# Optimization experiments

Hardware: AMD Instinct MI355X
Metric: run time of the kernel (lower is better)

Reference implementation:

```python
import jax, jax.numpy as jnp
import numpy as np

N, E, G, R = 65536, 524288, 1024, 512
D_IN, H, R_FEAT, NH, HD = 7, 128, 25, 4, 32
EPS = 1e-5


def setup_inputs() -> dict:
    key = jax.random.key(0)
    ks = jax.random.split(key, 16)
    f = lambda i, shape, s: jax.random.normal(ks[i], shape, jnp.float32) * s
    return {
        "x": jax.random.normal(ks[0], (N, D_IN), jnp.float32),
        "edge_index": jax.random.randint(ks[1], (2, E), 0, N),
        "batch": jnp.repeat(jnp.arange(G), N // G),  # 64 atoms per graph, sorted
        "per_residue_features": jax.random.normal(ks[2], (R, R_FEAT), jnp.float32),
        # GCN layer weights (PyG GCNConv: x @ W then normalized aggregation, + bias)
        "W0": f(3, (D_IN, H), 0.3), "b0": jnp.zeros(H, jnp.float32),
        "W1": f(4, (H, H), 0.1), "b1": jnp.zeros(H, jnp.float32),
        "W2": f(5, (H, H), 0.1), "b2": jnp.zeros(H, jnp.float32),
        # BatchNorm (eval mode, running stats)
        "bn_gamma": jnp.ones((3, H), jnp.float32),
        "bn_beta": jnp.zeros((3, H), jnp.float32),
        "bn_mean": f(6, (3, H), 0.1),
        "bn_var": jax.random.uniform(ks[7], (3, H), jnp.float32) + 0.5,
        # residue projection
        "res_W": f(8, (R_FEAT, H), 0.2), "res_b": jnp.zeros(H, jnp.float32),
        # MultiheadAttention packed in-proj (rows: q, k, v) and out-proj
        "in_W": f(9, (3 * H, H), 0.08), "in_b": jnp.zeros(3 * H, jnp.float32),
        "out_W": f(10, (H, H), 0.08), "out_b": jnp.zeros(H, jnp.float32),
        # classifier 128 -> 64 -> 1
        "cls_W1": f(11, (H, 64), 0.1), "cls_b1": jnp.zeros(64, jnp.float32),
        "cls_W2": f(12, (64, 1), 0.1), "cls_b2": jnp.zeros(1, jnp.float32),
    }


def reference(x, edge_index, batch, per_residue_features,
              W0, b0, W1, b1, W2, b2,
              bn_gamma, bn_beta, bn_mean, bn_var,
              res_W, res_b, in_W, in_b, out_W, out_b,
              cls_W1, cls_b1, cls_W2, cls_b2):
    src, dst = edge_index[0], edge_index[1]
    # GCN symmetric norm with self-loops: deg[i] = 1 + in-degree(i)
    deg = jnp.ones(N, x.dtype).at[dst].add(1.0)
    dinv = jax.lax.rsqrt(deg)
    enorm = (dinv[src] * dinv[dst])[:, None]      # [E,1]
    self_norm = (dinv * dinv)[:, None]            # [N,1]

    def gcn_bn_relu(h, W, b, i):
        m = h @ W                                  # [N,H]
        agg = m * self_norm
        agg = agg.at[dst].add(m[src] * enorm) + b
        y = bn_gamma[i] * (agg - bn_mean[i]) * jax.lax.rsqrt(bn_var[i] + EPS) + bn_beta[i]
        return jax.nn.relu(y)  # dropout is identity at inference

    h = gcn_bn_relu(x, W0, b0, 0)
    h = gcn_bn_relu(h, W1, b1, 1)
    h = gcn_bn_relu(h, W2, b2, 2)

    # shared residue KV (same for every graph) -> fused attention over all nodes
    res = per_residue_features @ res_W + res_b     # [R,H]
    Wq, Wk, Wv = jnp.split(in_W, 3, axis=0)
    bq, bk, bv = jnp.split(in_b, 3)
    q = (h @ Wq.T + bq).reshape(N, NH, HD)
    k = (res @ Wk.T + bk).reshape(R, NH, HD)
    v = (res @ Wv.T + bv).reshape(R, NH, HD)
    scores = jnp.einsum('nhd,rhd->nhr', q, k) / np.float32(np.sqrt(HD))
    attn = jax.nn.softmax(scores, axis=-1)         # [N,NH,R]
    o = jnp.einsum('nhr,rhd->nhd', attn, v).reshape(N, H)
    o = o @ out_W.T + out_b                        # [N,H]

    # per-graph mean pool (segment mean over batch ids)
    counts = jnp.zeros(G, o.dtype).at[batch].add(1.0)
    pooled = jnp.zeros((G, H), o.dtype).at[batch].add(o) / counts[:, None]

    hid = jax.nn.relu(pooled @ cls_W1 + cls_b1)
    logits = (hid @ cls_W2 + cls_b2)[:, 0]         # [G]
    return logits
```

## Files before the change

### kernel.cpp

```cpp
#include <hip/hip_runtime.h>
#include <math.h>

#define N_NODES 65536
#define N_EDGES 524288
#define N_GRAPHS 1024
#define H 128
#define R_RES 512
#define NH 4
#define HD 32
#define D_IN 7
#define EPS 1e-5f

typedef __attribute__((ext_vector_type(8))) short short8;
typedef __attribute__((ext_vector_type(4))) short short4v;
typedef __attribute__((ext_vector_type(4))) float f32x4;
typedef __attribute__((ext_vector_type(4))) unsigned uint4v;
typedef __attribute__((ext_vector_type(2))) unsigned uint2v;
typedef __attribute__((ext_vector_type(4))) unsigned short us4;

#if __has_builtin(__builtin_amdgcn_exp2f)
#define EXP2F __builtin_amdgcn_exp2f
#else
#define EXP2F exp2f
#endif
#if __has_builtin(__builtin_amdgcn_rcpf)
#define RCPF __builtin_amdgcn_rcpf
#else
#define RCPF(x) (1.0f/(x))
#endif

__device__ __forceinline__ f32x4 mfma_k16(short4v a, short4v b, f32x4 c){
#if defined(__HIP_DEVICE_COMPILE__)
  return __builtin_amdgcn_mfma_f32_16x16x16bf16_1k(a, b, c, 0, 0, 0);
#else
  (void)a; (void)b; return c;
#endif
}

__device__ __forceinline__ unsigned short rnd_bf16(float f){
  return (unsigned short)((__builtin_bit_cast(unsigned, f) + 0x8000u) >> 16);
}
__device__ __forceinline__ unsigned pk_bf16(float lo, float hi){
  unsigned a = __builtin_bit_cast(unsigned, lo) + 0x8000u;
  unsigned b = __builtin_bit_cast(unsigned, hi) + 0x8000u;
  return __builtin_amdgcn_perm(b, a, 0x07060302u);
}
__device__ __forceinline__ float bflo(unsigned u){ return __builtin_bit_cast(float, u << 16); }
__device__ __forceinline__ float bfhi(unsigned u){ return __builtin_bit_cast(float, u & 0xFFFF0000u); }

__device__ __forceinline__ void acc8(float* a, uint4v u, float wgt){
  a[0]=fmaf(bflo(u.x),wgt,a[0]); a[1]=fmaf(bfhi(u.x),wgt,a[1]);
  a[2]=fmaf(bflo(u.y),wgt,a[2]); a[3]=fmaf(bfhi(u.y),wgt,a[3]);
  a[4]=fmaf(bflo(u.z),wgt,a[4]); a[5]=fmaf(bfhi(u.z),wgt,a[5]);
  a[6]=fmaf(bflo(u.w),wgt,a[6]); a[7]=fmaf(bfhi(u.w),wgt,a[7]);
}

__global__ __launch_bounds__(256) void k_count(const int* __restrict__ dst, int* __restrict__ cnt, int E){
  int e = blockIdx.x*256 + threadIdx.x;
  if (e < E) atomicAdd(&cnt[dst[e]], 1);
}

__global__ __launch_bounds__(256) void k_part(const int* __restrict__ cnt, int* __restrict__ part){
  int i = blockIdx.x*256 + threadIdx.x;
  int v = cnt[i];
  #pragma unroll
  for (int off=1; off<64; off<<=1) v += __shfl_xor(v, off);
  __shared__ int red[4];
  if ((threadIdx.x & 63) == 0) red[threadIdx.x >> 6] = v;
  __syncthreads();
  if (threadIdx.x == 0) part[blockIdx.x] = red[0]+red[1]+red[2]+red[3];
}

__global__ __launch_bounds__(256) void k_scanp(int* __restrict__ part){
  __shared__ int s[256];
  int t = threadIdx.x;
  int v = part[t];
  s[t] = v;
  __syncthreads();
  for (int off=1; off<256; off<<=1){
    int u = (t >= off) ? s[t-off] : 0;
    __syncthreads();
    s[t] += u;
    __syncthreads();
  }
  part[t] = s[t] - v;
}

__global__ __launch_bounds__(256) void k_apply(const int* __restrict__ cnt, const int* __restrict__ part,
      int* __restrict__ csr_off, int* __restrict__ cursor, float* __restrict__ dinv){
  __shared__ int s[256];
  int b = blockIdx.x, t = threadIdx.x;
  int i = b*256 + t;
  int c = cnt[i];
  s[t] = c;
  __syncthreads();
  for (int off=1; off<256; off<<=1){
    int u = (t >= off) ? s[t-off] : 0;
    __syncthreads();
    s[t] += u;
    __syncthreads();
  }
  int o0 = part[b] + s[t] - c;
  csr_off[i] = o0;
  cursor[i] = o0;
  dinv[i] = rsqrtf(1.0f + (float)c);
  if (i == N_NODES-1) csr_off[N_NODES] = N_EDGES;
}

__global__ __launch_bounds__(256) void k_fill(const int* __restrict__ src, const int* __restrict__ dst,
      const float* __restrict__ dinv, int* __restrict__ cursor, int2* __restrict__ csr_ev, int E){
  int e = blockIdx.x*256 + threadIdx.x;
  if (e >= E) return;
  int s = src[e], d = dst[e];
  int p = atomicAdd(&cursor[d], 1);
  int2 rec;
  rec.x = s;
  rec.y = __builtin_bit_cast(int, dinv[s]*dinv[d]);
  csr_ev[p] = rec;
}

__global__ __launch_bounds__(256) void k_lin0(const float* __restrict__ x, const float* __restrict__ W0,
                                              unsigned short* __restrict__ out){
  int gid = blockIdx.x*256 + threadIdx.x;
  int l = threadIdx.x & 63;
  int n = __builtin_amdgcn_readfirstlane(gid >> 6);
  float a0 = 0.0f, a1 = 0.0f;
  #pragma unroll
  for (int k=0;k<D_IN;k++){
    float xv = x[(long)n*D_IN + k];
    float2 wv = *(const float2*)(W0 + k*H + 2*l);
    a0 = fmaf(xv, wv.x, a0); a1 = fmaf(xv, wv.y, a1);
  }
  *(unsigned*)(out + (long)n*H + 2*l) = pk_bf16(a0, a1);
}

__global__ __launch_bounds__(256) void k_gemm_mfma(const unsigned short* __restrict__ A,
      const float* __restrict__ Bsrc, const float* __restrict__ bias, void* __restrict__ Cout,
      int transB, int outMode){
  __shared__ unsigned short Bt[128][136];
  int tid = threadIdx.x;
  long rowBase = (long)blockIdx.x * 128;
  int w = tid >> 6, l = tid & 63;
  int lc = l & 15, q4 = l >> 4;

  if (transB){
    for (int i = tid; i < 4096; i += 256){
      int c = i >> 5, seg = i & 31;
      float4 v = *(const float4*)(Bsrc + (long)c*128 + seg*4);
      uint2 p; p.x = pk_bf16(v.x, v.y); p.y = pk_bf16(v.z, v.w);
      *(uint2*)&Bt[c][seg*4] = p;
    }
  } else {
    for (int i = tid; i < 4096; i += 256){
      int k = i >> 5, seg = i & 31;
      float4 v = *(const float4*)(Bsrc + (long)k*128 + seg*4);
      Bt[seg*4+0][k] = rnd_bf16(v.x); Bt[seg*4+1][k] = rnd_bf16(v.y);
      Bt[seg*4+2][k] = rnd_bf16(v.z); Bt[seg*4+3][k] = rnd_bf16(v.w);
    }
  }

  short8 af[2][4];
  #pragma unroll
  for (int rt=0;rt<2;rt++){
    long row = rowBase + w*32 + rt*16 + lc;
    #pragma unroll
    for (int kc=0;kc<4;kc++)
      af[rt][kc] = *(const short8*)(A + row*128 + kc*32 + q4*8);
  }

  f32x4 acc[2][8];
  #pragma unroll
  for (int rt=0;rt<2;rt++)
    #pragma unroll
    for (int ct=0;ct<8;ct++) acc[rt][ct] = (f32x4){0.f,0.f,0.f,0.f};

  __syncthreads();

  #pragma unroll
  for (int kc=0;kc<4;kc++){
    #pragma unroll
    for (int ct=0;ct<8;ct++){
      short8 bf = *(const short8*)&Bt[ct*16 + lc][kc*32 + q4*8];
      acc[0][ct] = __builtin_amdgcn_mfma_f32_16x16x32_bf16(af[0][kc], bf, acc[0][ct], 0,0,0);
      acc[1][ct] = __builtin_amdgcn_mfma_f32_16x16x32_bf16(af[1][kc], bf, acc[1][ct], 0,0,0);
    }
  }

  float bv[8];
  #pragma unroll
  for (int ct=0;ct<8;ct++) bv[ct] = bias ? bias[ct*16 + lc] : 0.0f;
  #pragma unroll
  for (int rt=0;rt<2;rt++){
    #pragma unroll
    for (int ct=0;ct<8;ct++){
      int col = ct*16 + lc;
      float vv[4];
      #pragma unroll
      for (int i=0;i<4;i++) vv[i] = acc[rt][ct][i] + bv[ct];
      long row0 = rowBase + w*32 + rt*16 + q4*4;
      if (outMode == 0){
        #pragma unroll
        for (int i=0;i<4;i++) ((unsigned short*)Cout)[(row0+i)*128 + col] = rnd_bf16(vv[i]);
      } else {
        #pragma unroll
        for (int i=0;i<4;i++) ((float*)Cout)[(row0+i)*128 + col] = vv[i];
      }
    }
  }
}

__global__ __launch_bounds__(256) void k_kv(const unsigned short* __restrict__ A,
      const float* __restrict__ inW, const float* __restrict__ inb,
      unsigned short* __restrict__ FK, unsigned short* __restrict__ FV){
  __shared__ unsigned short Bt[128][136];
  int tid = threadIdx.x;
  int blk = blockIdx.x;
  int isK = (blk < 4);
  const float* Bsrc = inW + (isK ? 128*128 : 256*128);
  const float* bias = inb + (isK ? 128 : 256);
  long rowBase = (long)(blk & 3) * 128;
  int w = tid >> 6, l = tid & 63;
  int lc = l & 15, q4 = l >> 4;

  for (int i = tid; i < 4096; i += 256){
    int c = i >> 5, seg = i & 31;
    float4 v = *(const float4*)(Bsrc + (long)c*128 + seg*4);
    uint2 p; p.x = pk_bf16(v.x, v.y); p.y = pk_bf16(v.z, v.w);
    *(uint2*)&Bt[c][seg*4] = p;
  }

  short8 af[2][4];
  #pragma unroll
  for (int rt=0;rt<2;rt++){
    long row = rowBase + w*32 + rt*16 + lc;
    #pragma unroll
    for (int kc=0;kc<4;kc++)
      af[rt][kc] = *(const short8*)(A + row*128 + kc*32 + q4*8);
  }

  f32x4 acc[2][8];
  #pragma unroll
  for (int rt=0;rt<2;rt++)
    #pragma unroll
    for (int ct=0;ct<8;ct++) acc[rt][ct] = (f32x4){0.f,0.f,0.f,0.f};

  __syncthreads();

  #pragma unroll
  for (int kc=0;kc<4;kc++){
    #pragma unroll
    for (int ct=0;ct<8;ct++){
      short8 bf = *(const short8*)&Bt[ct*16 + lc][kc*32 + q4*8];
      acc[0][ct] = __builtin_amdgcn_mfma_f32_16x16x32_bf16(af[0][kc], bf, acc[0][ct], 0,0,0);
      acc[1][ct] = __builtin_amdgcn_mfma_f32_16x16x32_bf16(af[1][kc], bf, acc[1][ct], 0,0,0);
    }
  }

  float bv[8];
  #pragma unroll
  for (int ct=0;ct<8;ct++) bv[ct] = bias[ct*16 + lc];
  #pragma unroll
  for (int rt=0;rt<2;rt++){
    long rc = ((blk & 3)*128 + w*32 + rt*16) >> 4;
    #pragma unroll
    for (int ct=0;ct<8;ct++){
      float vv[4];
      #pragma unroll
      for (int i=0;i<4;i++) vv[i] = acc[rt][ct][i] + bv[ct];
      int h = ct >> 1;
      if (isK){
        int q4d = (ct*2 + (lc >> 3)) & 3;
        long base = (long)h*16384 + rc*512 + q4d*128 + (q4*4)*8 + (lc & 7);
        #pragma unroll
        for (int i=0;i<4;i++) FK[base + i*8] = rnd_bf16(vv[i]);
      } else {
        long base = (long)h*16384 + rc*512 + q4*128 + lc*8 + (ct & 1)*4;
        us4 p = { rnd_bf16(vv[0]), rnd_bf16(vv[1]), rnd_bf16(vv[2]), rnd_bf16(vv[3]) };
        *(us4*)(FV + base) = p;
      }
    }
  }
}

__global__ __launch_bounds__(256) void k_agg(const unsigned short* __restrict__ m, const int* __restrict__ csr_off,
      const int2* __restrict__ csr_ev, const float* __restrict__ dinv,
      const float* __restrict__ b, const float* __restrict__ gamma, const float* __restrict__ beta,
      const float* __restrict__ mean, const float* __restrict__ var, unsigned short* __restrict__ out){
  int gt = blockIdx.x*256 + threadIdx.x;
  int li = gt & 15;
  int n = gt >> 4;
  int c = li*8;
  float dn = dinv[n], sn = dn*dn;
  float a[8];
  {
    uint4v u = *(const uint4v*)(m + (long)n*H + c);
    a[0]=bflo(u.x)*sn; a[1]=bfhi(u.x)*sn; a[2]=bflo(u.y)*sn; a[3]=bfhi(u.y)*sn;
    a[4]=bflo(u.z)*sn; a[5]=bfhi(u.z)*sn; a[6]=bflo(u.w)*sn; a[7]=bfhi(u.w)*sn;
  }
  int e0 = csr_off[n], e1 = csr_off[n+1];
  int e = e0;
  for (; e + 4 <= e1; e += 4){
    int2 p0 = csr_ev[e],   p1 = csr_ev[e+1];
    int2 p2 = csr_ev[e+2], p3 = csr_ev[e+3];
    uint4v u0 = *(const uint4v*)(m + (long)p0.x*H + c);
    uint4v u1 = *(const uint4v*)(m + (long)p1.x*H + c);
    uint4v u2 = *(const uint4v*)(m + (long)p2.x*H + c);
    uint4v u3 = *(const uint4v*)(m + (long)p3.x*H + c);
    acc8(a, u0, __builtin_bit_cast(float, p0.y));
    acc8(a, u1, __builtin_bit_cast(float, p1.y));
    acc8(a, u2, __builtin_bit_cast(float, p2.y));
    acc8(a, u3, __builtin_bit_cast(float, p3.y));
  }
  for (; e < e1; e++){
    int2 p0 = csr_ev[e];
    uint4v u0 = *(const uint4v*)(m + (long)p0.x*H + c);
    acc8(a, u0, __builtin_bit_cast(float, p0.y));
  }
  float4 g0 = *(const float4*)(gamma + c), g1 = *(const float4*)(gamma + c + 4);
  float4 v0 = *(const float4*)(var   + c), v1 = *(const float4*)(var   + c + 4);
  float4 b0 = *(const float4*)(b     + c), b1 = *(const float4*)(b     + c + 4);
  float4 m0 = *(const float4*)(mean  + c), m1 = *(const float4*)(mean  + c + 4);
  float4 t0 = *(const float4*)(beta  + c), t1 = *(const float4*)(beta  + c + 4);
  float r[8];
  r[0]=fmaxf(g0.x*rsqrtf(v0.x+EPS)*(a[0]+b0.x-m0.x)+t0.x, 0.f);
  r[1]=fmaxf(g0.y*rsqrtf(v0.y+EPS)*(a[1]+b0.y-m0.y)+t0.y, 0.f);
  r[2]=fmaxf(g0.z*rsqrtf(v0.z+EPS)*(a[2]+b0.z-m0.z)+t0.z, 0.f);
  r[3]=fmaxf(g0.w*rsqrtf(v0.w+EPS)*(a[3]+b0.w-m0.w)+t0.w, 0.f);
  r[4]=fmaxf(g1.x*rsqrtf(v1.x+EPS)*(a[4]+b1.x-m1.x)+t1.x, 0.f);
  r[5]=fmaxf(g1.y*rsqrtf(v1.y+EPS)*(a[5]+b1.y-m1.y)+t1.y, 0.f);
  r[6]=fmaxf(g1.z*rsqrtf(v1.z+EPS)*(a[6]+b1.z-m1.z)+t1.z, 0.f);
  r[7]=fmaxf(g1.w*rsqrtf(v1.w+EPS)*(a[7]+b1.w-m1.w)+t1.w, 0.f);
  uint4v p;
  p.x = pk_bf16(r[0],r[1]); p.y = pk_bf16(r[2],r[3]);
  p.z = pk_bf16(r[4],r[5]); p.w = pk_bf16(r[6],r[7]);
  *(uint4v*)(out + (long)n*H + c) = p;
}

__global__ __launch_bounds__(256,2) void k_gemm(const float* __restrict__ A, const float* __restrict__ B,
      const float* __restrict__ bias, void* __restrict__ C, int K, int transB, int outBf16){
  __shared__ float Bs[128][132];
  __shared__ float As[16][128];
  int tid = threadIdx.x;
  long rowBase = (long)blockIdx.x * 128;

  if (!transB){
    for (int idx = tid; idx < 128*128; idx += 256){
      int k = idx >> 7, c = idx & 127;
      Bs[k][c] = (k < K) ? B[(long)k*128 + c] : 0.0f;
    }
  } else {
    for (int idx = tid; idx < 128*128; idx += 256){
      int c = idx >> 7, k = idx & 127;
      Bs[k][c] = (k < K) ? B[(long)c*K + k] : 0.0f;
    }
  }

  float acc[8][8];
  #pragma unroll
  for (int i=0;i<8;i++)
    #pragma unroll
    for (int j=0;j<8;j++) acc[i][j] = 0.0f;

  int rg = tid >> 4, cg = tid & 15;
  int r0 = rg*8, c0 = cg*8;
  int srow = tid >> 1, skoff = (tid & 1)*8;
  const bool fast = ((K & 15) == 0);

  for (int k0 = 0; k0 < K; k0 += 16){
    __syncthreads();
    const float* ap = A + (rowBase + srow)*K + k0 + skoff;
    if (fast){
      float4 v0 = *(const float4*)(ap);
      float4 v1 = *(const float4*)(ap + 4);
      As[skoff+0][srow] = v0.x; As[skoff+1][srow] = v0.y;
      As[skoff+2][srow] = v0.z; As[skoff+3][srow] = v0.w;
      As[skoff+4][srow] = v1.x; As[skoff+5][srow] = v1.y;
      As[skoff+6][srow] = v1.z; As[skoff+7][srow] = v1.w;
    } else {
      #pragma unroll
      for (int j=0;j<8;j++){
        int kk = k0 + skoff + j;
        As[skoff+j][srow] = (kk < K) ? ap[j] : 0.0f;
      }
    }
    __syncthreads();
    #pragma unroll
    for (int k=0;k<16;k++){
      float4 a0 = *(const float4*)(&As[k][r0]);
      float4 a1 = *(const float4*)(&As[k][r0+4]);
      float4 b0 = *(const float4*)(&Bs[k0+k][c0]);
      float4 b1 = *(const float4*)(&Bs[k0+k][c0+4]);
      float a[8] = {a0.x,a0.y,a0.z,a0.w,a1.x,a1.y,a1.z,a1.w};
      float b[8] = {b0.x,b0.y,b0.z,b0.w,b1.x,b1.y,b1.z,b1.w};
      #pragma unroll
      for (int i=0;i<8;i++)
        #pragma unroll
        for (int j=0;j<8;j++)
          acc[i][j] = fmaf(a[i], b[j], acc[i][j]);
    }
  }

  #pragma unroll
  for (int i=0;i<8;i++){
    float o[8];
    #pragma unroll
    for (int j=0;j<8;j++) o[j] = acc[i][j] + (bias ? bias[c0+j] : 0.0f);
    long row = rowBase + r0 + i;
    if (outBf16){
      uint4v p;
      p.x = pk_bf16(o[0],o[1]); p.y = pk_bf16(o[2],o[3]);
      p.z = pk_bf16(o[4],o[5]); p.w = pk_bf16(o[6],o[7]);
      *(uint4v*)((unsigned short*)C + row*128 + c0) = p;
    } else {
      float* cp = (float*)C + row*128 + c0;
      *(float4*)cp = (float4){o[0],o[1],o[2],o[3]};
      *(float4*)(cp+4) = (float4){o[4],o[5],o[6],o[7]};
    }
  }
}

__global__ __launch_bounds__(256,4) void k_attn(const unsigned short* __restrict__ hb,
      const float* __restrict__ inW, const float* __restrict__ inb,
      const unsigned short* __restrict__ Kf, const unsigned short* __restrict__ Vf,
      unsigned short* __restrict__ obuf){
  int tid = threadIdx.x;
  int h = blockIdx.y;
  int w = tid >> 6, l = tid & 63;
  int lc = l & 15, q4 = l >> 4;
  long nb = (long)blockIdx.x*256 + w*64;
  const float scale = 0.25503489f;

  int srcA = lc + (q4 & 1)*32;
  int srcB = srcA + 16;
  bool hi = (q4 >> 1) != 0;

  short8 wq[2][4];
  #pragma unroll
  for (int t=0;t<2;t++){
    #pragma unroll
    for (int kc=0;kc<4;kc++){
      const float* wp = inW + (long)(h*32 + t*16 + lc)*128 + kc*32 + q4*8;
      float4 x0 = *(const float4*)wp;
      float4 x1 = *(const float4*)(wp+4);
      uint4v p; p.x = pk_bf16(x0.x,x0.y); p.y = pk_bf16(x0.z,x0.w);
      p.z = pk_bf16(x1.x,x1.y); p.w = pk_bf16(x1.z,x1.w);
      wq[t][kc] = __builtin_bit_cast(short8, p);
    }
  }
  float bq0[4], bq1[4];
  #pragma unroll
  for (int i=0;i<4;i++){ bq0[i] = inb[h*32 + q4*4 + i]; bq1[i] = inb[h*32 + 16 + q4*4 + i]; }

  short8 qB[4];
  #pragma unroll
  for (int nt=0;nt<4;nt++){
    short8 hf[4];
    #pragma unroll
    for (int kc=0;kc<4;kc++)
      hf[kc] = *(const short8*)(hb + (nb + nt*16 + lc)*128 + kc*32 + q4*8);
    f32x4 qa0 = (f32x4){0.f,0.f,0.f,0.f};
    f32x4 qa1 = (f32x4){0.f,0.f,0.f,0.f};
    #pragma unroll
    for (int kc=0;kc<4;kc++){
      qa0 = __builtin_amdgcn_mfma_f32_16x16x32_bf16(wq[0][kc], hf[kc], qa0, 0,0,0);
      qa1 = __builtin_amdgcn_mfma_f32_16x16x32_bf16(wq[1][kc], hf[kc], qa1, 0,0,0);
    }
    unsigned P0 = pk_bf16((qa0[0]+bq0[0])*scale, (qa0[1]+bq0[1])*scale);
    unsigned P1 = pk_bf16((qa0[2]+bq0[2])*scale, (qa0[3]+bq0[3])*scale);
    unsigned P2 = pk_bf16((qa1[0]+bq1[0])*scale, (qa1[1]+bq1[1])*scale);
    unsigned P3 = pk_bf16((qa1[2]+bq1[2])*scale, (qa1[3]+bq1[3])*scale);
    unsigned x0 = __shfl(P0, srcA), x1 = __shfl(P1, srcA), x2 = __shfl(P2, srcA), x3 = __shfl(P3, srcA);
    unsigned y0 = __shfl(P0, srcB), y1 = __shfl(P1, srcB), y2 = __shfl(P2, srcB), y3 = __shfl(P3, srcB);
    uint4v bp; bp.x = hi?x2:x0; bp.y = hi?x3:x1; bp.z = hi?y2:y0; bp.w = hi?y3:y1;
    qB[nt] = __builtin_bit_cast(short8, bp);
  }

  const short4v ones4 = {(short)0x3F80,(short)0x3F80,(short)0x3F80,(short)0x3F80};
  f32x4 oA[4], oB[4], os[4];
  #pragma unroll
  for (int nt=0;nt<4;nt++){
    oA[nt] = (f32x4){0.f,0.f,0.f,0.f};
    oB[nt] = (f32x4){0.f,0.f,0.f,0.f};
    os[nt] = (f32x4){0.f,0.f,0.f,0.f};
  }

  const unsigned short* Kp = Kf + (long)h*16384 + (long)l*8;
  const unsigned short* Vp = Vf + (long)h*16384 + (long)l*8;

  for (int rc = 0; rc < 32; rc++){
    short8 kf = *(const short8*)(Kp + rc*512);
    uint4v vv = *(const uint4v*)(Vp + rc*512);
    uint2v va = {vv.x, vv.y}, vb = {vv.z, vv.w};
    short4v vfA = __builtin_bit_cast(short4v, va);
    short4v vfB = __builtin_bit_cast(short4v, vb);
    #pragma unroll
    for (int nt=0;nt<4;nt++){
      f32x4 z = {0.f,0.f,0.f,0.f};
      f32x4 s = __builtin_amdgcn_mfma_f32_16x16x32_bf16(kf, qB[nt], z, 0,0,0);
      float e0 = EXP2F(s[0]), e1 = EXP2F(s[1]), e2 = EXP2F(s[2]), e3 = EXP2F(s[3]);
      uint2v pk2; pk2.x = pk_bf16(e0, e1); pk2.y = pk_bf16(e2, e3);
      short4v pf = __builtin_bit_cast(short4v, pk2);
      oA[nt] = mfma_k16(vfA,   pf, oA[nt]);
      oB[nt] = mfma_k16(vfB,   pf, oB[nt]);
      os[nt] = mfma_k16(ones4, pf, os[nt]);
    }
  }

  #pragma unroll
  for (int nt=0;nt<4;nt++){
    float inv = RCPF(os[nt][0]);
    long node = nb + nt*16 + lc;
    us4 a = { rnd_bf16(oA[nt][0]*inv), rnd_bf16(oA[nt][1]*inv),
              rnd_bf16(oA[nt][2]*inv), rnd_bf16(oA[nt][3]*inv) };
    us4 b = { rnd_bf16(oB[nt][0]*inv), rnd_bf16(oB[nt][1]*inv),
              rnd_bf16(oB[nt][2]*inv), rnd_bf16(oB[nt][3]*inv) };
    *(us4*)(obuf + node*128 + h*32 + q4*4) = a;
    *(us4*)(obuf + node*128 + h*32 + 16 + q4*4) = b;
  }
}

__global__ __launch_bounds__(256) void k_gemm_out(const unsigned short* __restrict__ A,
      const float* __restrict__ Bsrc, const float* __restrict__ bias,
      const float* __restrict__ W1, const float* __restrict__ b1,
      const float* __restrict__ W2, const float* __restrict__ b2, float* __restrict__ out){
  __shared__ unsigned short Bt[128][136];
  __shared__ float pools[4][128];
  __shared__ float pooled[2][128];
  int tid = threadIdx.x;
  long rowBase = (long)blockIdx.x * 128;
  int w = tid >> 6, l = tid & 63;
  int lc = l & 15, q4 = l >> 4;

  for (int i = tid; i < 4096; i += 256){
    int c = i >> 5, seg = i & 31;
    float4 v = *(const float4*)(Bsrc + (long)c*128 + seg*4);
    uint2 p; p.x = pk_bf16(v.x, v.y); p.y = pk_bf16(v.z, v.w);
    *(uint2*)&Bt[c][seg*4] = p;
  }

  short8 af[2][4];
  #pragma unroll
  for (int rt=0;rt<2;rt++){
    long row = rowBase + w*32 + rt*16 + lc;
    #pragma unroll
    for (int kc=0;kc<4;kc++)
      af[rt][kc] = *(const short8*)(A + row*128 + kc*32 + q4*8);
  }

  f32x4 acc[2][8];
  #pragma unroll
  for (int rt=0;rt<2;rt++)
    #pragma unroll
    for (int ct=0;ct<8;ct++) acc[rt][ct] = (f32x4){0.f,0.f,0.f,0.f};

  __syncthreads();

  #pragma unroll
  for (int kc=0;kc<4;kc++){
    #pragma unroll
    for (int ct=0;ct<8;ct++){
      short8 bf = *(const short8*)&Bt[ct*16 + lc][kc*32 + q4*8];
      acc[0][ct] = __builtin_amdgcn_mfma_f32_16x16x32_bf16(af[0][kc], bf, acc[0][ct], 0,0,0);
      acc[1][ct] = __builtin_amdgcn_mfma_f32_16x16x32_bf16(af[1][kc], bf, acc[1][ct], 0,0,0);
    }
  }

  #pragma unroll
  for (int ct=0;ct<8;ct++){
    float ps = acc[0][ct][0]+acc[0][ct][1]+acc[0][ct][2]+acc[0][ct][3]
             + acc[1][ct][0]+acc[1][ct][1]+acc[1][ct][2]+acc[1][ct][3];
    ps += __shfl_xor(ps, 16);
    ps += __shfl_xor(ps, 32);
    if (q4 == 0) pools[w][ct*16 + lc] = ps;
  }
  __syncthreads();

  if (tid < 128){
    int c = tid;
    pooled[0][c] = (pools[0][c] + pools[1][c]) * (1.0f/64.0f) + bias[c];
    pooled[1][c] = (pools[2][c] + pools[3][c]) * (1.0f/64.0f) + bias[c];
  }
  __syncthreads();

  if (tid < 128){
    int g = tid >> 6, tp = tid & 63;
    float hh = b1[tp];
    for (int c=0;c<128;c++) hh = fmaf(pooled[g][c], W1[c*64 + tp], hh);
    hh = fmaxf(hh, 0.0f);
    float v = hh * W2[tp];
    #pragma unroll
    for (int off=32; off>0; off>>=1) v += __shfl_down(v, off);
    if (tp == 0) out[blockIdx.x*2 + g] = v + b2[0];
  }
}

extern "C" void kernel_launch(void* const* d_in, const int* in_sizes, int n_in,
                              void* d_out, int out_size, void* d_ws, size_t ws_size,
                              hipStream_t stream){
  const float* x     = (const float*)d_in[0];
  const int*   ei    = (const int*)d_in[1];
  const float* perres= (const float*)d_in[3];
  const float* W0 = (const float*)d_in[4];
  const float* b0 = (const float*)d_in[5];
  const float* W1 = (const float*)d_in[6];  const float* b1 = (const float*)d_in[7];
  const float* W2 = (const float*)d_in[8];  const float* b2 = (const float*)d_in[9];
  const float* bng = (const float*)d_in[10]; const float* bnb = (const float*)d_in[11];
  const float* bnm = (const float*)d_in[12]; const float* bnv = (const float*)d_in[13];
  const float* resW = (const float*)d_in[14]; const float* resb = (const float*)d_in[15];
  const float* inW  = (const float*)d_in[16]; const float* inb  = (const float*)d_in[17];
  const float* outW = (const float*)d_in[18]; const float* outb = (const float*)d_in[19];
  const float* cW1 = (const float*)d_in[20]; const float* cb1 = (const float*)d_in[21];
  const float* cW2 = (const float*)d_in[22]; const float* cb2 = (const float*)d_in[23];
  float* out = (float*)d_out;

  char* ws = (char*)d_ws;
  size_t off = 0;
  auto alloc = [&](size_t bytes) -> char* {
    char* p = ws + off;
    off += (bytes + 255) & ~(size_t)255;
    return p;
  };
  float* dinv    = (float*)alloc((size_t)N_NODES*4);
  int*   cnt     = (int*)  alloc((size_t)N_NODES*4);
  int*   cursor  = (int*)  alloc((size_t)N_NODES*4);
  int*   csr_off = (int*)  alloc((size_t)(N_NODES+1)*4);
  int2*  csr_ev  = (int2*) alloc((size_t)N_EDGES*8);
  int*   part    = (int*)  alloc((size_t)256*4);
  unsigned short* mb  = (unsigned short*)alloc((size_t)N_NODES*H*2);
  unsigned short* hb  = (unsigned short*)alloc((size_t)N_NODES*H*2);
  unsigned short* resbuf = (unsigned short*)alloc((size_t)R_RES*H*2);
  unsigned short* Kfr = (unsigned short*)alloc((size_t)R_RES*H*2);
  unsigned short* Vfr = (unsigned short*)alloc((size_t)H*R_RES*2);
  if (off > ws_size) return;

  const int* srcI = ei;
  const int* dstI = ei + N_EDGES;

  (void)hipMemsetAsync(cnt, 0, (size_t)N_NODES*4, stream);
  k_count<<<N_EDGES/256, 256, 0, stream>>>(dstI, cnt, N_EDGES);
  k_part <<<N_NODES/256, 256, 0, stream>>>(cnt, part);
  k_scanp<<<1, 256, 0, stream>>>(part);
  k_apply<<<N_NODES/256, 256, 0, stream>>>(cnt, part, csr_off, cursor, dinv);
  k_fill <<<N_EDGES/256, 256, 0, stream>>>(srcI, dstI, dinv, cursor, csr_ev, N_EDGES);

  const int NB = N_NODES/128;
  const int AGB = N_NODES/16;
  k_lin0<<<N_NODES/4, 256, 0, stream>>>(x, W0, mb);
  k_agg<<<AGB, 256, 0, stream>>>(mb, csr_off, csr_ev, dinv, b0, bng,     bnb,     bnm,     bnv,     hb);
  k_gemm_mfma<<<NB, 256, 0, stream>>>(hb, W1, nullptr, mb, 0, 0);
  k_agg<<<AGB, 256, 0, stream>>>(mb, csr_off, csr_ev, dinv, b1, bng+128, bnb+128, bnm+128, bnv+128, hb);
  k_gemm_mfma<<<NB, 256, 0, stream>>>(hb, W2, nullptr, mb, 0, 0);
  k_agg<<<AGB, 256, 0, stream>>>(mb, csr_off, csr_ev, dinv, b2, bng+256, bnb+256, bnm+256, bnv+256, hb);

  k_gemm<<<R_RES/128, 256, 0, stream>>>(perres, resW, resb, resbuf, 25, 0, 1);
  k_kv<<<8, 256, 0, stream>>>(resbuf, inW, inb, Kfr, Vfr);

  dim3 agrid(N_NODES/256, NH);
  k_attn<<<agrid, 256, 0, stream>>>(hb, inW, inb, Kfr, Vfr, mb);

  k_gemm_out<<<NB, 256, 0, stream>>>(mb, outW, outb, cW1, cb1, cW2, cb2, out);
}
```

Baseline: 375.7 us.

## Aggregate raw 7-dim input before first linear layer in GCN layer 0

Reorders layer 0 so normalized neighbor aggregation runs on the 7-wide input features instead of the 128-wide projected features, using linearity (A(xW) = (Ax)W). A new kernel gathers and sums the fp32 input rows into a small buffer, and the linear kernel then applies W0, bias, BatchNorm and ReLU directly. This removes the 128-wide bf16 gather pass for the first layer and replaces it with a much smaller gather. The aggregation now stays in fp32 before projection, so rounding differs slightly, and the change adds a small extra buffer.

```diff
diff --git a/kernel.cpp b/kernel.cpp
--- a/kernel.cpp
+++ b/kernel.cpp
@@ -119,19 +119,55 @@
   csr_ev[p] = rec;
 }
 
-__global__ __launch_bounds__(256) void k_lin0(const float* __restrict__ x, const float* __restrict__ W0,
-                                              unsigned short* __restrict__ out){
+__global__ __launch_bounds__(256) void k_agg0(const float* __restrict__ x, const int* __restrict__ csr_off,
+      const int2* __restrict__ csr_ev, const float* __restrict__ dinv, float* __restrict__ xa){
+  int gt = blockIdx.x*256 + threadIdx.x;
+  int col = gt & 7;
+  int n = gt >> 3;
+  int cc = (col < D_IN) ? col : 0;
+  float dn = dinv[n];
+  float a = x[(long)n*D_IN + cc] * (dn*dn);
+  int e0 = csr_off[n], e1 = csr_off[n+1];
+  int e = e0;
+  for (; e + 2 <= e1; e += 2){
+    int2 p0 = csr_ev[e], p1 = csr_ev[e+1];
+    float v0 = x[(long)p0.x*D_IN + cc];
+    float v1 = x[(long)p1.x*D_IN + cc];
+    a = fmaf(v0, __builtin_bit_cast(float, p0.y), a);
+    a = fmaf(v1, __builtin_bit_cast(float, p1.y), a);
+  }
+  if (e < e1){
+    int2 p0 = csr_ev[e];
+    a = fmaf(x[(long)p0.x*D_IN + cc], __builtin_bit_cast(float, p0.y), a);
+  }
+  if (col < D_IN) xa[(long)n*D_IN + col] = a;
+}
+
+__global__ __launch_bounds__(256) void k_lin0(const float* __restrict__ xa, const float* __restrict__ W0,
+      const float* __restrict__ b0, const float* __restrict__ gamma, const float* __restrict__ beta,
+      const float* __restrict__ mean, const float* __restrict__ var, unsigned short* __restrict__ out){
   int gid = blockIdx.x*256 + threadIdx.x;
   int l = threadIdx.x & 63;
   int n = __builtin_amdgcn_readfirstlane(gid >> 6);
   float a0 = 0.0f, a1 = 0.0f;
   #pragma unroll
   for (int k=0;k<D_IN;k++){
-    float xv = x[(long)n*D_IN + k];
+    float xv = xa[(long)n*D_IN + k];
     float2 wv = *(const float2*)(W0 + k*H + 2*l);
     a0 = fmaf(xv, wv.x, a0); a1 = fmaf(xv, wv.y, a1);
   }
-  *(unsigned*)(out + (long)n*H + 2*l) = pk_bf16(a0, a1);
+  int c = 2*l;
+  float r0, r1;
+  {
+    float sc = gamma[c] * rsqrtf(var[c] + EPS);
+    r0 = fmaxf(sc*(a0 + b0[c] - mean[c]) + beta[c], 0.0f);
+  }
+  {
+    int c1 = c+1;
+    float sc = gamma[c1] * rsqrtf(var[c1] + EPS);
+    r1 = fmaxf(sc*(a1 + b0[c1] - mean[c1]) + beta[c1], 0.0f);
+  }
+  *(unsigned*)(out + (long)n*H + c) = pk_bf16(r0, r1);
 }
 
 __global__ __launch_bounds__(256) void k_gemm_mfma(const unsigned short* __restrict__ A,
@@ -626,6 +662,7 @@
   int*   csr_off = (int*)  alloc((size_t)(N_NODES+1)*4);
   int2*  csr_ev  = (int2*) alloc((size_t)N_EDGES*8);
   int*   part    = (int*)  alloc((size_t)256*4);
+  float* xa      = (float*)alloc((size_t)N_NODES*D_IN*4);
   unsigned short* mb  = (unsigned short*)alloc((size_t)N_NODES*H*2);
   unsigned short* hb  = (unsigned short*)alloc((size_t)N_NODES*H*2);
   unsigned short* resbuf = (unsigned short*)alloc((size_t)R_RES*H*2);
@@ -645,8 +682,8 @@
 
   const int NB = N_NODES/128;
   const int AGB = N_NODES/16;
-  k_lin0<<<N_NODES/4, 256, 0, stream>>>(x, W0, mb);
-  k_agg<<<AGB, 256, 0, stream>>>(mb, csr_off, csr_ev, dinv, b0, bng,     bnb,     bnm,     bnv,     hb);
+  k_agg0<<<N_NODES/32, 256, 0, stream>>>(x, csr_off, csr_ev, dinv, xa);
+  k_lin0<<<N_NODES/4, 256, 0, stream>>>(xa, W0, b0, bng, bnb, bnm, bnv, hb);
   k_gemm_mfma<<<NB, 256, 0, stream>>>(hb, W1, nullptr, mb, 0, 0);
   k_agg<<<AGB, 256, 0, stream>>>(mb, csr_off, csr_ev, dinv, b1, bng+128, bnb+128, bnm+128, bnv+128, hb);
   k_gemm_mfma<<<NB, 256, 0, stream>>>(hb, W2, nullptr, mb, 0, 0);
```

Measured after the change: 364.0 us. 3.1% less time.

## Aggregate raw 7-dim inputs before layer-0 projection; record atomic ranks for CSR fill

Applied to the files above, without the earlier changes.

Layer 0 now aggregates the 7-wide input features over the CSR neighbourhood first and then applies W0, bias, BatchNorm and ReLU in one kernel. This replaces a 128-wide bf16 gather plus a separate linear kernel with a much narrower gather. CSR construction keeps the rank returned by the counting atomic and uses offset plus rank in the fill, which removes the second atomic pass and the cursor array at the cost of an extra edge-sized buffer. The aggregation loop also gains an 8-way unrolled path to put more gathers in flight.

```diff
diff --git a/kernel.cpp b/kernel.cpp
--- a/kernel.cpp
+++ b/kernel.cpp
@@ -55,9 +55,10 @@
   a[6]=fmaf(bflo(u.w),wgt,a[6]); a[7]=fmaf(bfhi(u.w),wgt,a[7]);
 }
 
-__global__ __launch_bounds__(256) void k_count(const int* __restrict__ dst, int* __restrict__ cnt, int E){
+__global__ __launch_bounds__(256) void k_count(const int* __restrict__ dst, int* __restrict__ cnt,
+                                               int* __restrict__ rank, int E){
   int e = blockIdx.x*256 + threadIdx.x;
-  if (e < E) atomicAdd(&cnt[dst[e]], 1);
+  if (e < E) rank[e] = atomicAdd(&cnt[dst[e]], 1);
 }
 
 __global__ __launch_bounds__(256) void k_part(const int* __restrict__ cnt, int* __restrict__ part){
@@ -87,7 +88,7 @@
 }
 
 __global__ __launch_bounds__(256) void k_apply(const int* __restrict__ cnt, const int* __restrict__ part,
-      int* __restrict__ csr_off, int* __restrict__ cursor, float* __restrict__ dinv){
+      int* __restrict__ csr_off, float* __restrict__ dinv){
   __shared__ int s[256];
   int b = blockIdx.x, t = threadIdx.x;
   int i = b*256 + t;
@@ -102,36 +103,74 @@
   }
   int o0 = part[b] + s[t] - c;
   csr_off[i] = o0;
-  cursor[i] = o0;
   dinv[i] = rsqrtf(1.0f + (float)c);
   if (i == N_NODES-1) csr_off[N_NODES] = N_EDGES;
 }
 
 __global__ __launch_bounds__(256) void k_fill(const int* __restrict__ src, const int* __restrict__ dst,
-      const float* __restrict__ dinv, int* __restrict__ cursor, int2* __restrict__ csr_ev, int E){
+      const int* __restrict__ rank, const int* __restrict__ csr_off, const float* __restrict__ dinv,
+      int2* __restrict__ csr_ev, int E){
   int e = blockIdx.x*256 + threadIdx.x;
   if (e >= E) return;
   int s = src[e], d = dst[e];
-  int p = atomicAdd(&cursor[d], 1);
+  int p = csr_off[d] + rank[e];
   int2 rec;
   rec.x = s;
   rec.y = __builtin_bit_cast(int, dinv[s]*dinv[d]);
   csr_ev[p] = rec;
 }
 
-__global__ __launch_bounds__(256) void k_lin0(const float* __restrict__ x, const float* __restrict__ W0,
-                                              unsigned short* __restrict__ out){
-  int gid = blockIdx.x*256 + threadIdx.x;
-  int l = threadIdx.x & 63;
-  int n = __builtin_amdgcn_readfirstlane(gid >> 6);
-  float a0 = 0.0f, a1 = 0.0f;
-  #pragma unroll
-  for (int k=0;k<D_IN;k++){
-    float xv = x[(long)n*D_IN + k];
-    float2 wv = *(const float2*)(W0 + k*H + 2*l);
-    a0 = fmaf(xv, wv.x, a0); a1 = fmaf(xv, wv.y, a1);
-  }
-  *(unsigned*)(out + (long)n*H + 2*l) = pk_bf16(a0, a1);
+__global__ __launch_bounds__(256) void k_l0(const float* __restrict__ x, const int* __restrict__ csr_off,
+      const int2* __restrict__ csr_ev, const float* __restrict__ dinv,
+      const float* __restrict__ W0, const float* __restrict__ b0,
+      const float* __restrict__ gamma, const float* __restrict__ beta,
+      const float* __restrict__ mean, const float* __restrict__ var,
+      unsigned short* __restrict__ out){
+  __shared__ float xs[32][8];
+  int t = threadIdx.x;
+  long nb = (long)blockIdx.x*32;
+  {
+    int nl = t >> 3, col = t & 7;
+    int n = (int)nb + nl;
+    int cc = (col < D_IN) ? col : 0;
+    float dn = dinv[n];
+    float a = x[(long)n*D_IN + cc]*(dn*dn);
+    int e0 = csr_off[n], e1 = csr_off[n+1];
+    int e = e0;
+    for (; e + 2 <= e1; e += 2){
+      int2 p0 = csr_ev[e], p1 = csr_ev[e+1];
+      a = fmaf(x[(long)p0.x*D_IN + cc], __builtin_bit_cast(float, p0.y), a);
+      a = fmaf(x[(long)p1.x*D_IN + cc], __builtin_bit_cast(float, p1.y), a);
+    }
+    if (e < e1){
+      int2 p0 = csr_ev[e];
+      a = fmaf(x[(long)p0.x*D_IN + cc], __builtin_bit_cast(float, p0.y), a);
+    }
+    xs[nl][col] = a;
+  }
+  __syncthreads();
+  int w = t >> 6, l = t & 63;
+  int c = 2*l;
+  float sc0 = gamma[c]   * rsqrtf(var[c]   + EPS);
+  float sc1 = gamma[c+1] * rsqrtf(var[c+1] + EPS);
+  float d0 = sc0*(b0[c]   - mean[c])   + beta[c];
+  float d1 = sc1*(b0[c+1] - mean[c+1]) + beta[c+1];
+  float2 wv[D_IN];
+  #pragma unroll
+  for (int k=0;k<D_IN;k++) wv[k] = *(const float2*)(W0 + k*H + c);
+  #pragma unroll
+  for (int i=0;i<8;i++){
+    int nl = w*8 + i;
+    float a0 = 0.0f, a1 = 0.0f;
+    #pragma unroll
+    for (int k=0;k<D_IN;k++){
+      float xv = xs[nl][k];
+      a0 = fmaf(xv, wv[k].x, a0); a1 = fmaf(xv, wv[k].y, a1);
+    }
+    float r0 = fmaxf(fmaf(sc0, a0, d0), 0.0f);
+    float r1 = fmaxf(fmaf(sc1, a1, d1), 0.0f);
+    *(unsigned*)(out + (nb + nl)*H + c) = pk_bf16(r0, r1);
+  }
 }
 
 __global__ __launch_bounds__(256) void k_gemm_mfma(const unsigned short* __restrict__ A,
@@ -299,9 +338,28 @@
   }
   int e0 = csr_off[n], e1 = csr_off[n+1];
   int e = e0;
+  for (; e + 8 <= e1; e += 8){
+    int2 p0 = csr_ev[e],   p1 = csr_ev[e+1], p2 = csr_ev[e+2], p3 = csr_ev[e+3];
+    int2 p4 = csr_ev[e+4], p5 = csr_ev[e+5], p6 = csr_ev[e+6], p7 = csr_ev[e+7];
+    uint4v u0 = *(const uint4v*)(m + (long)p0.x*H + c);
+    uint4v u1 = *(const uint4v*)(m + (long)p1.x*H + c);
+    uint4v u2 = *(const uint4v*)(m + (long)p2.x*H + c);
+    uint4v u3 = *(const uint4v*)(m + (long)p3.x*H + c);
+    uint4v u4 = *(const uint4v*)(m + (long)p4.x*H + c);
+    uint4v u5 = *(const uint4v*)(m + (long)p5.x*H + c);
+    uint4v u6 = *(const uint4v*)(m + (long)p6.x*H + c);
+    uint4v u7 = *(const uint4v*)(m + (long)p7.x*H + c);
+    acc8(a, u0, __builtin_bit_cast(float, p0.y));
+    acc8(a, u1, __builtin_bit_cast(float, p1.y));
+    acc8(a, u2, __builtin_bit_cast(float, p2.y));
+    acc8(a, u3, __builtin_bit_cast(float, p3.y));
+    acc8(a, u4, __builtin_bit_cast(float, p4.y));
+    acc8(a, u5, __builtin_bit_cast(float, p5.y));
+    acc8(a, u6, __builtin_bit_cast(float, p6.y));
+    acc8(a, u7, __builtin_bit_cast(float, p7.y));
+  }
   for (; e + 4 <= e1; e += 4){
-    int2 p0 = csr_ev[e],   p1 = csr_ev[e+1];
-    int2 p2 = csr_ev[e+2], p3 = csr_ev[e+3];
+    int2 p0 = csr_ev[e], p1 = csr_ev[e+1], p2 = csr_ev[e+2], p3 = csr_ev[e+3];
     uint4v u0 = *(const uint4v*)(m + (long)p0.x*H + c);
     uint4v u1 = *(const uint4v*)(m + (long)p1.x*H + c);
     uint4v u2 = *(const uint4v*)(m + (long)p2.x*H + c);
@@ -622,8 +680,8 @@
   };
   float* dinv    = (float*)alloc((size_t)N_NODES*4);
   int*   cnt     = (int*)  alloc((size_t)N_NODES*4);
-  int*   cursor  = (int*)  alloc((size_t)N_NODES*4);
   int*   csr_off = (int*)  alloc((size_t)(N_NODES+1)*4);
+  int*   rankb   = (int*)  alloc((size_t)N_EDGES*4);
   int2*  csr_ev  = (int2*) alloc((size_t)N_EDGES*8);
   int*   part    = (int*)  alloc((size_t)256*4);
   unsigned short* mb  = (unsigned short*)alloc((size_t)N_NODES*H*2);
@@ -637,16 +695,15 @@
   const int* dstI = ei + N_EDGES;
 
   (void)hipMemsetAsync(cnt, 0, (size_t)N_NODES*4, stream);
-  k_count<<<N_EDGES/256, 256, 0, stream>>>(dstI, cnt, N_EDGES);
+  k_count<<<N_EDGES/256, 256, 0, stream>>>(dstI, cnt, rankb, N_EDGES);
   k_part <<<N_NODES/256, 256, 0, stream>>>(cnt, part);
   k_scanp<<<1, 256, 0, stream>>>(part);
-  k_apply<<<N_NODES/256, 256, 0, stream>>>(cnt, part, csr_off, cursor, dinv);
-  k_fill <<<N_EDGES/256, 256, 0, stream>>>(srcI, dstI, dinv, cursor, csr_ev, N_EDGES);
+  k_apply<<<N_NODES/256, 256, 0, stream>>>(cnt, part, csr_off, dinv);
+  k_fill <<<N_EDGES/256, 256, 0, stream>>>(srcI, dstI, rankb, csr_off, dinv, csr_ev, N_EDGES);
 
   const int NB = N_NODES/128;
   const int AGB = N_NODES/16;
-  k_lin0<<<N_NODES/4, 256, 0, stream>>>(x, W0, mb);
-  k_agg<<<AGB, 256, 0, stream>>>(mb, csr_off, csr_ev, dinv, b0, bng,     bnb,     bnm,     bnv,     hb);
+  k_l0<<<N_NODES/32, 256, 0, stream>>>(x, csr_off, csr_ev, dinv, W0, b0, bng, bnb, bnm, bnv, hb);
   k_gemm_mfma<<<NB, 256, 0, stream>>>(hb, W1, nullptr, mb, 0, 0);
   k_agg<<<AGB, 256, 0, stream>>>(mb, csr_off, csr_ev, dinv, b1, bng+128, bnb+128, bnm+128, bnv+128, hb);
   k_gemm_mfma<<<NB, 256, 0, stream>>>(hb, W2, nullptr, mb, 0, 0);
```

Measured after the change: 338.9 us. -9.8%, faster.
